# Performance work log

Measured on AMD Instinct MI355X. Metric: run time of the kernel, lower is better.

Reference implementation:

```python
import jax, jax.numpy as jnp
import numpy as np

B, T, D = 1024, 512, 128  # batch, history length, embedding = num_units


def setup_inputs() -> dict:
    key = jax.random.key(0)
    ks = jax.random.split(key, 5)
    s = 1.0 / np.sqrt(2 * D)
    return {
        "rnn_input": jax.random.normal(ks[0], (B, T, D), jnp.float32),
        "att_score": jax.random.uniform(ks[1], (B, T, 1), jnp.float32),
        "gate_kernel": jax.random.normal(ks[2], (2 * D, 2 * D), jnp.float32) * s,
        "gate_bias": jnp.ones((2 * D,), jnp.float32),  # TF GRUCell init: gate bias = 1.0
        "cand_kernel": jax.random.normal(ks[3], (2 * D, D), jnp.float32) * s,
        "cand_bias": jnp.zeros((D,), jnp.float32),
        "sequence_length": jax.random.randint(ks[4], (B, 1), 1, T + 1, jnp.int32),
    }


def reference(rnn_input, att_score, gate_kernel, gate_bias, cand_kernel, cand_bias, sequence_length):
    # AUGRU (VecAttGRUCell) dynamic_rnn, return_sequence=True
    Bv, Tv, Dv = rnn_input.shape
    lens = sequence_length.reshape(Bv)                      # tf.squeeze
    x_t = jnp.transpose(rnn_input, (1, 0, 2))               # [T,B,D]
    a_t = jnp.transpose(att_score, (1, 0, 2))               # [T,B,1]
    mask = (jnp.arange(Tv)[:, None] < lens[None, :])[..., None]  # [T,B,1] bool
    h0 = jnp.zeros((Bv, Dv), rnn_input.dtype)

    def step(h, xs):
        x, a, m = xs
        gi = jnp.concatenate([x, h], -1) @ gate_kernel + gate_bias
        r, u = jnp.split(jax.nn.sigmoid(gi), 2, axis=-1)
        c = jnp.tanh(jnp.concatenate([x, r * h], -1) @ cand_kernel + cand_bias)
        u = (1.0 - a) * u                                   # attention-gated update
        new_h = u * h + (1.0 - u) * c
        h_next = jnp.where(m, new_h, h)                     # state copy-through past length
        out = jnp.where(m, new_h, 0.0)                      # dynamic_rnn zeros past length
        return h_next, out

    _, outs = jax.lax.scan(step, h0, (x_t, a_t, mask))
    return jnp.transpose(outs, (1, 0, 2))                   # [B,T,D]
```

## Files before the change

### kernel.cpp

```cpp
#include <hip/hip_runtime.h>
#include <hip/hip_bf16.h>


#define Bn 1024
#define Tn 512
#define Dn 128

typedef __attribute__((ext_vector_type(8))) short short8;
typedef __attribute__((ext_vector_type(4))) short short4v;
typedef __attribute__((ext_vector_type(4))) float f32x4;

#define HS 132
#define BS 136

__device__ __forceinline__ short f2bf(float f) {
    __hip_bfloat16 h = __float2bfloat16(f);
    return __builtin_bit_cast(short, h);
}
__device__ __forceinline__ float sigmoidf_(float x) {
    float e = __expf(-x);
    return __builtin_amdgcn_rcpf(1.0f + e);
}
__device__ __forceinline__ float tanhf_(float x) {
    float e = __expf(-2.0f * x);
    return 2.0f * __builtin_amdgcn_rcpf(1.0f + e) - 1.0f;
}

__device__ __forceinline__ void barrier_lds() {
    __builtin_amdgcn_sched_barrier(0);
    asm volatile("s_waitcnt lgkmcnt(0)" ::: "memory");
    __builtin_amdgcn_s_barrier();
    __builtin_amdgcn_sched_barrier(0);
}

__launch_bounds__(512, 2)
__global__ void augru_kernel(const float* __restrict__ X,
                             const float* __restrict__ ATT,
                             const float* __restrict__ GK,
                             const float* __restrict__ GB,
                             const float* __restrict__ CK,
                             const float* __restrict__ CB,
                             const int*   __restrict__ SL,
                             float* __restrict__ OUT) {
    __shared__ short hb [16 * BS];
    __shared__ short rhb[16 * BS];
    __shared__ short xb [2][16 * BS];
    __shared__ float hf [16 * HS];
    __shared__ float ub [16 * HS];
    __shared__ float abuf[2][16];
    __shared__ int   lenbuf[16];

    const int tid  = threadIdx.x;
    const int wid  = tid >> 6;
    const int lane = tid & 63;
    const int lm   = lane & 15;
    const int q    = lane >> 4;
    const int b0   = blockIdx.x * 16;

    short8 fgx[2][4], fgh[2][4], fcx[4], fch[4];
    const int gcolb = 32 * wid + lm;
    const int ccol  = 16 * wid + lm;
#pragma unroll
    for (int ns = 0; ns < 2; ++ns) {
        const int col = gcolb + 16 * ns;
#pragma unroll
        for (int ks = 0; ks < 4; ++ks) {
            short8 vx, vh;
#pragma unroll
            for (int j = 0; j < 8; ++j) {
                const int k = ks * 32 + q * 8 + j;
                vx[j] = f2bf(GK[k * 256 + col]);
                vh[j] = f2bf(GK[(128 + k) * 256 + col]);
            }
            fgx[ns][ks] = vx; fgh[ns][ks] = vh;
        }
    }
#pragma unroll
    for (int ks = 0; ks < 4; ++ks) {
        short8 vx, vh;
#pragma unroll
        for (int j = 0; j < 8; ++j) {
            const int k = ks * 32 + q * 8 + j;
            vx[j] = f2bf(CK[k * 128 + ccol]);
            vh[j] = f2bf(CK[(128 + k) * 128 + ccol]);
        }
        fcx[ks] = vx; fch[ks] = vh;
    }
    const float gb0 = GB[gcolb];
    const float gb1 = GB[gcolb + 16];
    const float cb  = CB[ccol];

    for (int i = tid; i < 16 * HS; i += 512) hf[i] = 0.0f;
    for (int i = tid; i < 16 * BS; i += 512) hb[i] = 0;
    if (tid < 16) {
        lenbuf[tid]  = SL[b0 + tid];
        abuf[0][tid] = ATT[(size_t)(b0 + tid) * Tn];
    }
    const int prow = tid >> 5;
    const int pcol = (tid & 31) * 4;
    {
        float4 v = *(const float4*)(X + ((size_t)(b0 + prow) * Tn + 0) * Dn + pcol);
        short4v s; s[0] = f2bf(v.x); s[1] = f2bf(v.y); s[2] = f2bf(v.z); s[3] = f2bf(v.w);
        *(short4v*)&xb[0][prow * BS + pcol] = s;
    }
    __syncthreads();

    int len_i[4];
#pragma unroll
    for (int i = 0; i < 4; ++i) len_i[i] = lenbuf[q * 4 + i];

    for (int t = 0; t < Tn; ++t) {
        const int cur = t & 1, nxt = cur ^ 1;

        const int tp = (t + 1 < Tn) ? t + 1 : Tn - 1;
        float4 xpre = *(const float4*)(X + ((size_t)(b0 + prow) * Tn + tp) * Dn + pcol);
        float  apre = (tid < 16) ? ATT[(size_t)(b0 + tid) * Tn + tp] : 0.0f;

        short8 ax[4], ah[4];
#pragma unroll
        for (int ks = 0; ks < 4; ++ks) {
            ax[ks] = *(const short8*)&xb[cur][lm * BS + ks * 32 + q * 8];
            ah[ks] = *(const short8*)&hb[lm * BS + ks * 32 + q * 8];
        }

        f32x4 g0 = {0.f, 0.f, 0.f, 0.f}, g1 = {0.f, 0.f, 0.f, 0.f};
#pragma unroll
        for (int ks = 0; ks < 4; ++ks) {
            g0 = __builtin_amdgcn_mfma_f32_16x16x32_bf16(ah[ks], fgh[0][ks], g0, 0, 0, 0);
            g1 = __builtin_amdgcn_mfma_f32_16x16x32_bf16(ah[ks], fgh[1][ks], g1, 0, 0, 0);
            g0 = __builtin_amdgcn_mfma_f32_16x16x32_bf16(ax[ks], fgx[0][ks], g0, 0, 0, 0);
            g1 = __builtin_amdgcn_mfma_f32_16x16x32_bf16(ax[ks], fgx[1][ks], g1, 0, 0, 0);
        }

        if (wid < 4) {
#pragma unroll
            for (int ns = 0; ns < 2; ++ns) {
                const int col = 32 * wid + 16 * ns + lm;
                const float bias = ns ? gb1 : gb0;
                const f32x4 gg = ns ? g1 : g0;
#pragma unroll
                for (int i = 0; i < 4; ++i) {
                    const int row = q * 4 + i;
                    const float r = sigmoidf_(gg[i] + bias);
                    rhb[row * BS + col] = f2bf(r * hf[row * HS + col]);
                }
            }
        } else {
#pragma unroll
            for (int ns = 0; ns < 2; ++ns) {
                const int cu = 32 * (wid - 4) + 16 * ns + lm;
                const float bias = ns ? gb1 : gb0;
                const f32x4 gg = ns ? g1 : g0;
#pragma unroll
                for (int i = 0; i < 4; ++i) {
                    const int row = q * 4 + i;
                    const float u = sigmoidf_(gg[i] + bias);
                    ub[row * HS + cu] = (1.0f - abuf[cur][row]) * u;
                }
            }
        }
        barrier_lds();

        f32x4 cc = {0.f, 0.f, 0.f, 0.f};
#pragma unroll
        for (int ks = 0; ks < 4; ++ks) {
            short8 arh = *(const short8*)&rhb[lm * BS + ks * 32 + q * 8];
            cc = __builtin_amdgcn_mfma_f32_16x16x32_bf16(arh, fch[ks], cc, 0, 0, 0);
            cc = __builtin_amdgcn_mfma_f32_16x16x32_bf16(ax[ks], fcx[ks], cc, 0, 0, 0);
        }

#pragma unroll
        for (int i = 0; i < 4; ++i) {
            const int row = q * 4 + i;
            const float cv   = tanhf_(cc[i] + cb);
            const float up   = ub[row * HS + ccol];
            const float hold = hf[row * HS + ccol];
            const float hn   = up * hold + (1.0f - up) * cv;
            const bool valid = (t < len_i[i]);
            const float hnext = valid ? hn : hold;
            OUT[((size_t)(b0 + row) * Tn + t) * Dn + ccol] = valid ? hn : 0.0f;
            hf[row * HS + ccol] = hnext;
            hb[row * BS + ccol] = f2bf(hnext);
        }

        {
            short4v s; s[0] = f2bf(xpre.x); s[1] = f2bf(xpre.y);
                       s[2] = f2bf(xpre.z); s[3] = f2bf(xpre.w);
            *(short4v*)&xb[nxt][prow * BS + pcol] = s;
            if (tid < 16) abuf[nxt][tid] = apre;
        }
        barrier_lds();
    }
}

extern "C" void kernel_launch(void* const* d_in, const int* in_sizes, int n_in,
                              void* d_out, int out_size, void* d_ws, size_t ws_size,
                              hipStream_t stream) {
    (void)in_sizes; (void)n_in; (void)d_ws; (void)ws_size; (void)out_size;
    const float* X   = (const float*)d_in[0];
    const float* ATT = (const float*)d_in[1];
    const float* GK  = (const float*)d_in[2];
    const float* GB  = (const float*)d_in[3];
    const float* CK  = (const float*)d_in[4];
    const float* CB  = (const float*)d_in[5];
    const int*   SL  = (const int*)d_in[6];
    float* OUT = (float*)d_out;

    augru_kernel<<<dim3(Bn / 16), dim3(512), 0, stream>>>(X, ATT, GK, GB, CK, CB, SL, OUT);
}
```

Baseline: 629.9 us.

## Software-pipeline input projections one timestep ahead of the recurrent MFMAs

Computes the x-dependent gate and candidate MFMA products for step t+1 during step t and carries them as accumulators, so the dependent chain after each barrier only holds the h-dependent MFMAs. The x prefetch moves two steps ahead and the loop is unrolled by two with a macro to alternate the register sets. This adds accumulator registers and a deeper prefetch buffer schedule, which may pressure occupancy under the 512x2 launch bounds.

After: 614.7 us. 2.4% less time.

```diff
diff --git a/kernel.cpp b/kernel.cpp
--- a/kernel.cpp
+++ b/kernel.cpp
@@ -32,6 +32,8 @@
     __builtin_amdgcn_s_barrier();
     __builtin_amdgcn_sched_barrier(0);
 }
+
+#define MFMA_(a, b, c) __builtin_amdgcn_mfma_f32_16x16x32_bf16((a), (b), (c), 0, 0, 0)
 
 __launch_bounds__(512, 2)
 __global__ void augru_kernel(const float* __restrict__ X,
@@ -109,88 +111,120 @@
 #pragma unroll
     for (int i = 0; i < 4; ++i) len_i[i] = lenbuf[q * 4 + i];
 
-    for (int t = 0; t < Tn; ++t) {
-        const int cur = t & 1, nxt = cur ^ 1;
-
-        const int tp = (t + 1 < Tn) ? t + 1 : Tn - 1;
-        float4 xpre = *(const float4*)(X + ((size_t)(b0 + prow) * Tn + tp) * Dn + pcol);
-        float  apre = (tid < 16) ? ATT[(size_t)(b0 + tid) * Tn + tp] : 0.0f;
-
-        short8 ax[4], ah[4];
+    f32x4 gxA0 = {0.f,0.f,0.f,0.f}, gxA1 = {0.f,0.f,0.f,0.f}, cxA = {0.f,0.f,0.f,0.f};
+    f32x4 gxB0, gxB1, cxB;
+    {
+        short8 ax0[4];
+#pragma unroll
+        for (int ks = 0; ks < 4; ++ks)
+            ax0[ks] = *(const short8*)&xb[0][lm * BS + ks * 32 + q * 8];
 #pragma unroll
         for (int ks = 0; ks < 4; ++ks) {
-            ax[ks] = *(const short8*)&xb[cur][lm * BS + ks * 32 + q * 8];
-            ah[ks] = *(const short8*)&hb[lm * BS + ks * 32 + q * 8];
+            gxA0 = MFMA_(ax0[ks], fgx[0][ks], gxA0);
+            gxA1 = MFMA_(ax0[ks], fgx[1][ks], gxA1);
+            cxA  = MFMA_(ax0[ks], fcx[ks],  cxA);
         }
-
-        f32x4 g0 = {0.f, 0.f, 0.f, 0.f}, g1 = {0.f, 0.f, 0.f, 0.f};
-#pragma unroll
-        for (int ks = 0; ks < 4; ++ks) {
-            g0 = __builtin_amdgcn_mfma_f32_16x16x32_bf16(ah[ks], fgh[0][ks], g0, 0, 0, 0);
-            g1 = __builtin_amdgcn_mfma_f32_16x16x32_bf16(ah[ks], fgh[1][ks], g1, 0, 0, 0);
-            g0 = __builtin_amdgcn_mfma_f32_16x16x32_bf16(ax[ks], fgx[0][ks], g0, 0, 0, 0);
-            g1 = __builtin_amdgcn_mfma_f32_16x16x32_bf16(ax[ks], fgx[1][ks], g1, 0, 0, 0);
-        }
-
-        if (wid < 4) {
-#pragma unroll
-            for (int ns = 0; ns < 2; ++ns) {
-                const int col = 32 * wid + 16 * ns + lm;
-                const float bias = ns ? gb1 : gb0;
-                const f32x4 gg = ns ? g1 : g0;
-#pragma unroll
-                for (int i = 0; i < 4; ++i) {
-                    const int row = q * 4 + i;
-                    const float r = sigmoidf_(gg[i] + bias);
-                    rhb[row * BS + col] = f2bf(r * hf[row * HS + col]);
-                }
-            }
-        } else {
-#pragma unroll
-            for (int ns = 0; ns < 2; ++ns) {
-                const int cu = 32 * (wid - 4) + 16 * ns + lm;
-                const float bias = ns ? gb1 : gb0;
-                const f32x4 gg = ns ? g1 : g0;
-#pragma unroll
-                for (int i = 0; i < 4; ++i) {
-                    const int row = q * 4 + i;
-                    const float u = sigmoidf_(gg[i] + bias);
-                    ub[row * HS + cu] = (1.0f - abuf[cur][row]) * u;
-                }
-            }
-        }
-        barrier_lds();
-
-        f32x4 cc = {0.f, 0.f, 0.f, 0.f};
-#pragma unroll
-        for (int ks = 0; ks < 4; ++ks) {
-            short8 arh = *(const short8*)&rhb[lm * BS + ks * 32 + q * 8];
-            cc = __builtin_amdgcn_mfma_f32_16x16x32_bf16(arh, fch[ks], cc, 0, 0, 0);
-            cc = __builtin_amdgcn_mfma_f32_16x16x32_bf16(ax[ks], fcx[ks], cc, 0, 0, 0);
-        }
-
-#pragma unroll
-        for (int i = 0; i < 4; ++i) {
-            const int row = q * 4 + i;
-            const float cv   = tanhf_(cc[i] + cb);
-            const float up   = ub[row * HS + ccol];
-            const float hold = hf[row * HS + ccol];
-            const float hn   = up * hold + (1.0f - up) * cv;
-            const bool valid = (t < len_i[i]);
-            const float hnext = valid ? hn : hold;
-            OUT[((size_t)(b0 + row) * Tn + t) * Dn + ccol] = valid ? hn : 0.0f;
-            hf[row * HS + ccol] = hnext;
-            hb[row * BS + ccol] = f2bf(hnext);
-        }
-
-        {
-            short4v s; s[0] = f2bf(xpre.x); s[1] = f2bf(xpre.y);
-                       s[2] = f2bf(xpre.z); s[3] = f2bf(xpre.w);
-            *(short4v*)&xb[nxt][prow * BS + pcol] = s;
-            if (tid < 16) abuf[nxt][tid] = apre;
-        }
-        barrier_lds();
-    }
+        float4 v = *(const float4*)(X + ((size_t)(b0 + prow) * Tn + 1) * Dn + pcol);
+        short4v s; s[0] = f2bf(v.x); s[1] = f2bf(v.y); s[2] = f2bf(v.z); s[3] = f2bf(v.w);
+        *(short4v*)&xb[1][prow * BS + pcol] = s;
+    }
+    __syncthreads();
+
+#define STEP_BODY(t, GIN0, GIN1, CIN, GOUT0, GOUT1, COUT)                         \
+    {                                                                             \
+        const int cur = (t) & 1, nxt = cur ^ 1;                                   \
+        const int tp1 = ((t) + 1 < Tn) ? (t) + 1 : Tn - 1;                        \
+        const int tp2 = ((t) + 2 < Tn) ? (t) + 2 : Tn - 1;                        \
+        float4 xpre = *(const float4*)(X + ((size_t)(b0 + prow) * Tn + tp2) * Dn + pcol); \
+        float  apre = (tid < 16) ? ATT[(size_t)(b0 + tid) * Tn + tp1] : 0.0f;     \
+                                  \
+        short8 axn[4], ah[4];                                                     \
+        _Pragma("unroll")                                                         \
+        for (int ks = 0; ks < 4; ++ks) {                                          \
+            axn[ks] = *(const short8*)&xb[nxt][lm * BS + ks * 32 + q * 8];        \
+            ah[ks]  = *(const short8*)&hb[lm * BS + ks * 32 + q * 8];             \
+        }                                                                         \
+         \
+        f32x4 g0 = GIN0, g1 = GIN1;                                               \
+        f32x4 ngx0 = {0.f,0.f,0.f,0.f}, ngx1 = {0.f,0.f,0.f,0.f};                 \
+        f32x4 ncx  = {0.f,0.f,0.f,0.f};                                           \
+        _Pragma("unroll")                                                         \
+        for (int ks = 0; ks < 4; ++ks) {                                          \
+            g0 = MFMA_(ah[ks], fgh[0][ks], g0);                                   \
+            g1 = MFMA_(ah[ks], fgh[1][ks], g1);                                   \
+        }                                                                         \
+        _Pragma("unroll")                                                         \
+        for (int ks = 0; ks < 4; ++ks) {                                          \
+            ngx0 = MFMA_(axn[ks], fgx[0][ks], ngx0);                              \
+            ngx1 = MFMA_(axn[ks], fgx[1][ks], ngx1);                              \
+            ncx  = MFMA_(axn[ks], fcx[ks],  ncx);                                 \
+        }                                                                         \
+                            \
+        if (wid < 4) {                                         \
+            _Pragma("unroll")                                                     \
+            for (int ns = 0; ns < 2; ++ns) {                                      \
+                const int col = 32 * wid + 16 * ns + lm;                          \
+                const float bias = ns ? gb1 : gb0;                                \
+                const f32x4 gg = ns ? g1 : g0;                                    \
+                _Pragma("unroll")                                                 \
+                for (int i = 0; i < 4; ++i) {                                     \
+                    const int row = q * 4 + i;                                    \
+                    const float r = sigmoidf_(gg[i] + bias);                      \
+                    rhb[row * BS + col] = f2bf(r * hf[row * HS + col]);           \
+                }                                                                 \
+            }                                                                     \
+        } else {                                             \
+            _Pragma("unroll")                                                     \
+            for (int ns = 0; ns < 2; ++ns) {                                      \
+                const int cu = 32 * (wid - 4) + 16 * ns + lm;                     \
+                const float bias = ns ? gb1 : gb0;                                \
+                const f32x4 gg = ns ? g1 : g0;                                    \
+                _Pragma("unroll")                                                 \
+                for (int i = 0; i < 4; ++i) {                                     \
+                    const int row = q * 4 + i;                                    \
+                    const float u = sigmoidf_(gg[i] + bias);                      \
+                    ub[row * HS + cu] = (1.0f - abuf[cur][row]) * u;              \
+                }                                                                 \
+            }                                                                     \
+        }                                                                         \
+        barrier_lds();                                                            \
+                               \
+        f32x4 cc = CIN;                                                           \
+        _Pragma("unroll")                                                         \
+        for (int ks = 0; ks < 4; ++ks) {                                          \
+            short8 arh = *(const short8*)&rhb[lm * BS + ks * 32 + q * 8];         \
+            cc = MFMA_(arh, fch[ks], cc);                                         \
+        }                                                                         \
+                                                           \
+        _Pragma("unroll")                                                         \
+        for (int i = 0; i < 4; ++i) {                                             \
+            const int row = q * 4 + i;                                            \
+            const float cv   = tanhf_(cc[i] + cb);                                \
+            const float up   = ub[row * HS + ccol];                               \
+            const float hold = hf[row * HS + ccol];                               \
+            const float hn   = up * hold + (1.0f - up) * cv;                      \
+            const bool valid = ((t) < len_i[i]);                                  \
+            const float hnext = valid ? hn : hold;                                \
+            OUT[((size_t)(b0 + row) * Tn + (t)) * Dn + ccol] = valid ? hn : 0.0f; \
+            hf[row * HS + ccol] = hnext;                                          \
+            hb[row * BS + ccol] = f2bf(hnext);                                    \
+        }                                                                         \
+                            \
+        {                                                                         \
+            short4v s; s[0] = f2bf(xpre.x); s[1] = f2bf(xpre.y);                  \
+                       s[2] = f2bf(xpre.z); s[3] = f2bf(xpre.w);                  \
+            *(short4v*)&xb[cur][prow * BS + pcol] = s;                            \
+            if (tid < 16) abuf[nxt][tid] = apre;                                  \
+        }                                                                         \
+        barrier_lds();                                                            \
+        GOUT0 = ngx0; GOUT1 = ngx1; COUT = ncx;                                   \
+    }
+
+    for (int t = 0; t < Tn; t += 2) {
+        STEP_BODY(t,     gxA0, gxA1, cxA, gxB0, gxB1, cxB)
+        STEP_BODY(t + 1, gxB0, gxB1, cxB, gxA0, gxA1, cxA)
+    }
+#undef STEP_BODY
 }
 
 extern "C" void kernel_launch(void* const* d_in, const int* in_sizes, int n_in,
```

## Interleave two batch groups per block and precompute next-step input projections

Applied to the files above, without the earlier changes.

Each block now handles two 16-row batch groups, A and B, and runs their recurrences staggered so one group's matmuls overlap the other's activations and state update. The input-side projections (x@Wx for gates and candidate) are computed one step ahead, which shortens the dependent chain per step. Activations use exp2 with pre-scaled biases, and bf16 packing uses v_cvt_pk_bf16. The grid is halved to 32 blocks, which leaves most of the GPU's CUs idle in exchange for more instruction-level overlap within each block.

New measurement: 1.155 ms. 83.4% more time.

```diff
diff --git a/kernel.cpp b/kernel.cpp
--- a/kernel.cpp
+++ b/kernel.cpp
@@ -7,31 +7,31 @@
 #define Dn 128
 
 typedef __attribute__((ext_vector_type(8))) short short8;
-typedef __attribute__((ext_vector_type(4))) short short4v;
 typedef __attribute__((ext_vector_type(4))) float f32x4;
 
 #define HS 132
 #define BS 136
+
+#define NL2E  (-1.4426950408889634f)
+#define N2L2E (-2.8853900817779268f)
 
 __device__ __forceinline__ short f2bf(float f) {
     __hip_bfloat16 h = __float2bfloat16(f);
     return __builtin_bit_cast(short, h);
 }
-__device__ __forceinline__ float sigmoidf_(float x) {
-    float e = __expf(-x);
-    return __builtin_amdgcn_rcpf(1.0f + e);
-}
-__device__ __forceinline__ float tanhf_(float x) {
-    float e = __expf(-2.0f * x);
-    return 2.0f * __builtin_amdgcn_rcpf(1.0f + e) - 1.0f;
-}
-
+__device__ __forceinline__ unsigned cvt_pk_bf16(float a, float b) {
+    unsigned r;
+    asm("v_cvt_pk_bf16_f32 %0, %1, %2" : "=v"(r) : "v"(a), "v"(b));
+    return r;
+}
 __device__ __forceinline__ void barrier_lds() {
     __builtin_amdgcn_sched_barrier(0);
     asm volatile("s_waitcnt lgkmcnt(0)" ::: "memory");
     __builtin_amdgcn_s_barrier();
     __builtin_amdgcn_sched_barrier(0);
 }
+
+#define MFMA_(a, b, c) __builtin_amdgcn_mfma_f32_16x16x32_bf16((a), (b), (c), 0, 0, 0)
 
 __launch_bounds__(512, 2)
 __global__ void augru_kernel(const float* __restrict__ X,
@@ -42,20 +42,21 @@
                              const float* __restrict__ CB,
                              const int*   __restrict__ SL,
                              float* __restrict__ OUT) {
-    __shared__ short hb [16 * BS];
-    __shared__ short rhb[16 * BS];
-    __shared__ short xb [2][16 * BS];
-    __shared__ float hf [16 * HS];
-    __shared__ float ub [16 * HS];
-    __shared__ float abuf[2][16];
-    __shared__ int   lenbuf[16];
+    __shared__ short hbA [16 * BS], hbB [16 * BS];
+    __shared__ short rhbA[16 * BS], rhbB[16 * BS];
+    __shared__ short xbA [16 * BS], xbB [16 * BS];
+    __shared__ float hfA [16 * HS], hfB [16 * HS];
+    __shared__ float ubA [16 * HS], ubB [16 * HS];
+    __shared__ float abufA[2][16], abufB[2][16];
+    __shared__ int   lenbufA[16], lenbufB[16];
 
     const int tid  = threadIdx.x;
     const int wid  = tid >> 6;
     const int lane = tid & 63;
     const int lm   = lane & 15;
     const int q    = lane >> 4;
-    const int b0   = blockIdx.x * 16;
+    const int b0A  = blockIdx.x * 32;
+    const int b0B  = b0A + 16;
 
     short8 fgx[2][4], fgh[2][4], fcx[4], fch[4];
     const int gcolb = 32 * wid + lm;
@@ -86,111 +87,180 @@
         }
         fcx[ks] = vx; fch[ks] = vh;
     }
-    const float gb0 = GB[gcolb];
-    const float gb1 = GB[gcolb + 16];
-    const float cb  = CB[ccol];
-
-    for (int i = tid; i < 16 * HS; i += 512) hf[i] = 0.0f;
-    for (int i = tid; i < 16 * BS; i += 512) hb[i] = 0;
+    const float pb0 = GB[gcolb]      * NL2E;
+    const float pb1 = GB[gcolb + 16] * NL2E;
+    const float cbp = CB[ccol]       * N2L2E;
+
+    for (int i = tid; i < 16 * HS; i += 512) { hfA[i] = 0.0f; hfB[i] = 0.0f; }
+    for (int i = tid; i < 16 * BS; i += 512) { hbA[i] = 0;    hbB[i] = 0;    }
     if (tid < 16) {
-        lenbuf[tid]  = SL[b0 + tid];
-        abuf[0][tid] = ATT[(size_t)(b0 + tid) * Tn];
+        lenbufA[tid]  = SL[b0A + tid];
+        lenbufB[tid]  = SL[b0B + tid];
+        abufA[0][tid] = ATT[(size_t)(b0A + tid) * Tn];
+        abufB[0][tid] = ATT[(size_t)(b0B + tid) * Tn];
     }
     const int prow = tid >> 5;
     const int pcol = (tid & 31) * 4;
+
+#define STAGE_X(XBg, B0g, tt) {                                                     \
+        float4 v_ = *(const float4*)(X + ((size_t)((B0g) + prow) * Tn + (tt)) * Dn + pcol); \
+        uint2 pp_; pp_.x = cvt_pk_bf16(v_.x, v_.y); pp_.y = cvt_pk_bf16(v_.z, v_.w); \
+        *(uint2*)&XBg[prow * BS + pcol] = pp_; }
+
+    STAGE_X(xbA, b0A, 0)
+    STAGE_X(xbB, b0B, 0)
+    __syncthreads();
+
+    int lenA_i[4], lenB_i[4];
+#pragma unroll
+    for (int i = 0; i < 4; ++i) { lenA_i[i] = lenbufA[q * 4 + i]; lenB_i[i] = lenbufB[q * 4 + i]; }
+
+    f32x4 gxA0 = {0,0,0,0}, gxA1 = {0,0,0,0}, cxA = {0,0,0,0};
+    f32x4 gxB0 = {0,0,0,0}, gxB1 = {0,0,0,0}, cxB = {0,0,0,0};
+    f32x4 ccA, ccB, g0A, g1A, g0B, g1B;
+    float4 xpreA, xpreB; float apreA, apreB;
     {
-        float4 v = *(const float4*)(X + ((size_t)(b0 + prow) * Tn + 0) * Dn + pcol);
-        short4v s; s[0] = f2bf(v.x); s[1] = f2bf(v.y); s[2] = f2bf(v.z); s[3] = f2bf(v.w);
-        *(short4v*)&xb[0][prow * BS + pcol] = s;
+        short8 fa[4], fb[4];
+#pragma unroll
+        for (int ks = 0; ks < 4; ++ks) {
+            fa[ks] = *(const short8*)&xbA[lm * BS + ks * 32 + q * 8];
+            fb[ks] = *(const short8*)&xbB[lm * BS + ks * 32 + q * 8];
+        }
+#pragma unroll
+        for (int ks = 0; ks < 4; ++ks) {
+            gxA0 = MFMA_(fa[ks], fgx[0][ks], gxA0);
+            gxA1 = MFMA_(fa[ks], fgx[1][ks], gxA1);
+            cxA  = MFMA_(fa[ks], fcx[ks],  cxA);
+            gxB0 = MFMA_(fb[ks], fgx[0][ks], gxB0);
+            gxB1 = MFMA_(fb[ks], fgx[1][ks], gxB1);
+            cxB  = MFMA_(fb[ks], fcx[ks],  cxB);
+        }
     }
     __syncthreads();
-
-    int len_i[4];
-#pragma unroll
-    for (int i = 0; i < 4; ++i) len_i[i] = lenbuf[q * 4 + i];
+    STAGE_X(xbA, b0A, 1)
+    STAGE_X(xbB, b0B, 1)
+    __syncthreads();
+
+#define P1MFMA(HBg, XBg, GX0, GX1, CXg, CCg, G0, G1, XPREg, APREg, B0g, t)          \
+    {                                                                               \
+        const int tp1 = ((t) + 1 < Tn) ? (t) + 1 : Tn - 1;                          \
+        const int tp2 = ((t) + 2 < Tn) ? (t) + 2 : Tn - 1;                          \
+        XPREg = *(const float4*)(X + ((size_t)((B0g) + prow) * Tn + tp2) * Dn + pcol); \
+        APREg = (tid < 16) ? ATT[(size_t)((B0g) + tid) * Tn + tp1] : 0.0f;          \
+        short8 axn[4], ah[4];                                                       \
+        _Pragma("unroll")                                                           \
+        for (int ks = 0; ks < 4; ++ks) {                                            \
+            axn[ks] = *(const short8*)&XBg[lm * BS + ks * 32 + q * 8];              \
+            ah[ks]  = *(const short8*)&HBg[lm * BS + ks * 32 + q * 8];              \
+        }                                                                           \
+        G0 = GX0; G1 = GX1; CCg = CXg;                                              \
+        f32x4 n0 = {0,0,0,0}, n1 = {0,0,0,0}, n2 = {0,0,0,0};                       \
+        _Pragma("unroll")                                                           \
+        for (int ks = 0; ks < 4; ++ks) {                                            \
+            G0 = MFMA_(ah[ks], fgh[0][ks], G0);                                     \
+            G1 = MFMA_(ah[ks], fgh[1][ks], G1);                                     \
+            n0 = MFMA_(axn[ks], fgx[0][ks], n0);                                    \
+            n1 = MFMA_(axn[ks], fgx[1][ks], n1);                                    \
+            n2 = MFMA_(axn[ks], fcx[ks],  n2);                                      \
+        }                                                                           \
+        GX0 = n0; GX1 = n1; CXg = n2;                                               \
+    }
+
+#define ACT(RHBg, UBg, HFg, ABUFg, G0, G1, t)                                       \
+    {                                                                               \
+        if (wid < 4) {                                                  \
+            const int col0 = 32 * wid + lm;                                         \
+            _Pragma("unroll")                                                       \
+            for (int i = 0; i < 4; ++i) {                                           \
+                const int row = q * 4 + i;                                          \
+                const float e0 = __builtin_amdgcn_exp2f(fmaf(G0[i], NL2E, pb0));    \
+                const float e1 = __builtin_amdgcn_exp2f(fmaf(G1[i], NL2E, pb1));    \
+                const float rh0 = __builtin_amdgcn_rcpf(1.0f + e0) * HFg[row * HS + col0];      \
+                const float rh1 = __builtin_amdgcn_rcpf(1.0f + e1) * HFg[row * HS + col0 + 16]; \
+                const unsigned p = cvt_pk_bf16(rh0, rh1);                           \
+                RHBg[row * BS + col0]      = (short)p;                              \
+                RHBg[row * BS + col0 + 16] = (short)(p >> 16);                      \
+            }                                                                       \
+        } else {                                                        \
+            const int cu0 = 32 * (wid - 4) + lm;                                    \
+            float am[4];                                                            \
+            _Pragma("unroll")                                                       \
+            for (int i = 0; i < 4; ++i) am[i] = 1.0f - ABUFg[(t) & 1][q * 4 + i];   \
+            _Pragma("unroll")                                                       \
+            for (int i = 0; i < 4; ++i) {                                           \
+                const int row = q * 4 + i;                                          \
+                const float e0 = __builtin_amdgcn_exp2f(fmaf(G0[i], NL2E, pb0));    \
+                const float e1 = __builtin_amdgcn_exp2f(fmaf(G1[i], NL2E, pb1));    \
+                UBg[row * HS + cu0]      = am[i] * __builtin_amdgcn_rcpf(1.0f + e0); \
+                UBg[row * HS + cu0 + 16] = am[i] * __builtin_amdgcn_rcpf(1.0f + e1); \
+            }                                                                       \
+        }                                                                           \
+    }
+
+#define P2MFMA(RHBg, CCg)                                                           \
+    {                                                                               \
+        _Pragma("unroll")                                                           \
+        for (int ks = 0; ks < 4; ++ks) {                                            \
+            short8 arh = *(const short8*)&RHBg[lm * BS + ks * 32 + q * 8];          \
+            CCg = MFMA_(arh, fch[ks], CCg);                                         \
+        }                                                                           \
+    }
+
+#define UPD(HBg, XBg, HFg, UBg, ABUFg, LEN, CCg, XPREg, APREg, B0g, t)              \
+    {                                                                               \
+        float hxv[4];                                                               \
+        _Pragma("unroll")                                                           \
+        for (int i = 0; i < 4; ++i) {                                               \
+            const int row = q * 4 + i;                                              \
+            const float e  = __builtin_amdgcn_exp2f(fmaf(CCg[i], N2L2E, cbp));      \
+            const float cv = fmaf(2.0f, __builtin_amdgcn_rcpf(1.0f + e), -1.0f);    \
+            const float up   = UBg[row * HS + ccol];                                \
+            const float hold = HFg[row * HS + ccol];                                \
+            const float hn   = fmaf(up, hold - cv, cv);                             \
+            const bool valid = ((t) < LEN[i]);                                      \
+            const float hnext = valid ? hn : hold;                                  \
+            OUT[((size_t)((B0g) + row) * Tn + (t)) * Dn + ccol] = valid ? hn : 0.0f; \
+            HFg[row * HS + ccol] = hnext;                                           \
+            hxv[i] = hnext;                                                         \
+        }                                                                           \
+        {                                                                           \
+            const unsigned pA_ = cvt_pk_bf16(hxv[0], hxv[1]);                       \
+            const unsigned pB_ = cvt_pk_bf16(hxv[2], hxv[3]);                       \
+            HBg[(q * 4 + 0) * BS + ccol] = (short)pA_;                              \
+            HBg[(q * 4 + 1) * BS + ccol] = (short)(pA_ >> 16);                      \
+            HBg[(q * 4 + 2) * BS + ccol] = (short)pB_;                              \
+            HBg[(q * 4 + 3) * BS + ccol] = (short)(pB_ >> 16);                      \
+        }                                                                           \
+        {                                                                           \
+            uint2 pp_;                                                              \
+            pp_.x = cvt_pk_bf16(XPREg.x, XPREg.y);                                  \
+            pp_.y = cvt_pk_bf16(XPREg.z, XPREg.w);                                  \
+            *(uint2*)&XBg[prow * BS + pcol] = pp_;                                  \
+            if (tid < 16) ABUFg[((t) + 1) & 1][tid] = APREg;                        \
+        }                                                                           \
+    }
+
+    P1MFMA(hbB, xbB, gxB0, gxB1, cxB, ccB, g0B, g1B, xpreB, apreB, b0B, 0)
+    ACT(rhbB, ubB, hfB, abufB, g0B, g1B, 0)
+    barrier_lds();
 
     for (int t = 0; t < Tn; ++t) {
-        const int cur = t & 1, nxt = cur ^ 1;
-
-        const int tp = (t + 1 < Tn) ? t + 1 : Tn - 1;
-        float4 xpre = *(const float4*)(X + ((size_t)(b0 + prow) * Tn + tp) * Dn + pcol);
-        float  apre = (tid < 16) ? ATT[(size_t)(b0 + tid) * Tn + tp] : 0.0f;
-
-        short8 ax[4], ah[4];
-#pragma unroll
-        for (int ks = 0; ks < 4; ++ks) {
-            ax[ks] = *(const short8*)&xb[cur][lm * BS + ks * 32 + q * 8];
-            ah[ks] = *(const short8*)&hb[lm * BS + ks * 32 + q * 8];
-        }
-
-        f32x4 g0 = {0.f, 0.f, 0.f, 0.f}, g1 = {0.f, 0.f, 0.f, 0.f};
-#pragma unroll
-        for (int ks = 0; ks < 4; ++ks) {
-            g0 = __builtin_amdgcn_mfma_f32_16x16x32_bf16(ah[ks], fgh[0][ks], g0, 0, 0, 0);
-            g1 = __builtin_amdgcn_mfma_f32_16x16x32_bf16(ah[ks], fgh[1][ks], g1, 0, 0, 0);
-            g0 = __builtin_amdgcn_mfma_f32_16x16x32_bf16(ax[ks], fgx[0][ks], g0, 0, 0, 0);
-            g1 = __builtin_amdgcn_mfma_f32_16x16x32_bf16(ax[ks], fgx[1][ks], g1, 0, 0, 0);
-        }
-
-        if (wid < 4) {
-#pragma unroll
-            for (int ns = 0; ns < 2; ++ns) {
-                const int col = 32 * wid + 16 * ns + lm;
-                const float bias = ns ? gb1 : gb0;
-                const f32x4 gg = ns ? g1 : g0;
-#pragma unroll
-                for (int i = 0; i < 4; ++i) {
-                    const int row = q * 4 + i;
-                    const float r = sigmoidf_(gg[i] + bias);
-                    rhb[row * BS + col] = f2bf(r * hf[row * HS + col]);
-                }
-            }
-        } else {
-#pragma unroll
-            for (int ns = 0; ns < 2; ++ns) {
-                const int cu = 32 * (wid - 4) + 16 * ns + lm;
-                const float bias = ns ? gb1 : gb0;
-                const f32x4 gg = ns ? g1 : g0;
-#pragma unroll
-                for (int i = 0; i < 4; ++i) {
-                    const int row = q * 4 + i;
-                    const float u = sigmoidf_(gg[i] + bias);
-                    ub[row * HS + cu] = (1.0f - abuf[cur][row]) * u;
-                }
-            }
-        }
+        P1MFMA(hbA, xbA, gxA0, gxA1, cxA, ccA, g0A, g1A, xpreA, apreA, b0A, t)
+        P2MFMA(rhbB, ccB)
+        ACT(rhbA, ubA, hfA, abufA, g0A, g1A, t)
+        UPD(hbB, xbB, hfB, ubB, abufB, lenB_i, ccB, xpreB, apreB, b0B, t)
         barrier_lds();
-
-        f32x4 cc = {0.f, 0.f, 0.f, 0.f};
-#pragma unroll
-        for (int ks = 0; ks < 4; ++ks) {
-            short8 arh = *(const short8*)&rhb[lm * BS + ks * 32 + q * 8];
-            cc = __builtin_amdgcn_mfma_f32_16x16x32_bf16(arh, fch[ks], cc, 0, 0, 0);
-            cc = __builtin_amdgcn_mfma_f32_16x16x32_bf16(ax[ks], fcx[ks], cc, 0, 0, 0);
-        }
-
-#pragma unroll
-        for (int i = 0; i < 4; ++i) {
-            const int row = q * 4 + i;
-            const float cv   = tanhf_(cc[i] + cb);
-            const float up   = ub[row * HS + ccol];
-            const float hold = hf[row * HS + ccol];
-            const float hn   = up * hold + (1.0f - up) * cv;
-            const bool valid = (t < len_i[i]);
-            const float hnext = valid ? hn : hold;
-            OUT[((size_t)(b0 + row) * Tn + t) * Dn + ccol] = valid ? hn : 0.0f;
-            hf[row * HS + ccol] = hnext;
-            hb[row * BS + ccol] = f2bf(hnext);
-        }
-
-        {
-            short4v s; s[0] = f2bf(xpre.x); s[1] = f2bf(xpre.y);
-                       s[2] = f2bf(xpre.z); s[3] = f2bf(xpre.w);
-            *(short4v*)&xb[nxt][prow * BS + pcol] = s;
-            if (tid < 16) abuf[nxt][tid] = apre;
-        }
+        P2MFMA(rhbA, ccA)
+        P1MFMA(hbB, xbB, gxB0, gxB1, cxB, ccB, g0B, g1B, xpreB, apreB, b0B, t + 1)
+        UPD(hbA, xbA, hfA, ubA, abufA, lenA_i, ccA, xpreA, apreA, b0A, t)
+        ACT(rhbB, ubB, hfB, abufB, g0B, g1B, t + 1)
         barrier_lds();
     }
+#undef P1MFMA
+#undef ACT
+#undef P2MFMA
+#undef UPD
+#undef STAGE_X
 }
 
 extern "C" void kernel_launch(void* const* d_in, const int* in_sizes, int n_in,
@@ -206,5 +276,5 @@
     const int*   SL  = (const int*)d_in[6];
     float* OUT = (float*)d_out;
 
-    augru_kernel<<<dim3(Bn / 16), dim3(512), 0, stream>>>(X, ATT, GK, GB, CK, CB, SL, OUT);
-}
+    augru_kernel<<<dim3(Bn / 32), dim3(512), 0, stream>>>(X, ATT, GK, GB, CK, CB, SL, OUT);
+}
```
